# Kernel optimization log

Measured on AMD Instinct MI355X. Metric: run time of the kernel, lower is better.

## Reference

```python
import jax, jax.numpy as jnp
import numpy as np

B, D, H, O, E = 65536, 128, 256, 8, 8  # batch, input_dim, hidden_dim, output_dim, n_phases


def setup_inputs() -> dict:
    key = jax.random.key(0)
    ks = jax.random.split(key, 6)
    scale = 0.05
    x = jax.random.normal(ks[0], (B, D), dtype=jnp.float32)
    phases = jax.random.randint(ks[1], (B,), 0, E, dtype=jnp.int32)
    Ws = jax.random.normal(ks[2], (D, H), dtype=jnp.float32) * scale  # shared Linear weight (transposed)
    bs = jnp.zeros((H,), dtype=jnp.float32)
    W1 = jax.random.normal(ks[3], (E, H, H), dtype=jnp.float32) * scale  # per-head first Linear
    b1 = jnp.zeros((E, H), dtype=jnp.float32)
    W2 = jax.random.normal(ks[4], (E, H, O), dtype=jnp.float32) * scale  # per-head second Linear
    b2 = jnp.zeros((E, O), dtype=jnp.float32)
    return {"x": x, "phases": phases, "Ws": Ws, "bs": bs,
            "W1": W1, "b1": b1, "W2": W2, "b2": b2}


def reference(x, phases, Ws, bs, W1, b1, W2, b2):
    # shared trunk: Linear + ReLU
    h = jax.nn.relu(x @ Ws + bs)                                # [B, H]
    # run every head on every sample (dense grouped GEMM), then gather the
    # per-sample routed head. NOTE: no activation between the two head Linears,
    # matching nn.Sequential(Linear, Linear) in the source.
    h1 = jnp.einsum('bh,ehk->ebk', h, W1) + b1[:, None, :]      # [E, B, H]
    y = jnp.einsum('ebk,eko->ebo', h1, W2) + b2[:, None, :]     # [E, B, O]
    q = y[phases, jnp.arange(x.shape[0])]                       # [B, O] routed select
    return q
```

## Files before the change

### kernel.cpp

```cpp
#include <hip/hip_runtime.h>
#include <hip/hip_bf16.h>
#include <cstdint>


using bf16x8 = __attribute__((ext_vector_type(8))) __bf16;
using f32x4  = __attribute__((ext_vector_type(4))) float;

__device__ __forceinline__ unsigned short bf16b(float f) {
    __bf16 h = (__bf16)f;
    return __builtin_bit_cast(unsigned short, h);
}
__device__ __forceinline__ unsigned pack2(float a, float b) {
    return (unsigned)bf16b(a) | ((unsigned)bf16b(b) << 16);
}

__global__ void prep_kernel(const float* __restrict__ Ws,
                            const float* __restrict__ b1,
                            const float* __restrict__ W1,
                            const float* __restrict__ W2,
                            const float* __restrict__ b2,
                            uint4* __restrict__ wsP,
                            unsigned short* __restrict__ wfP,
                            float* __restrict__ bfuse) {
    const int bid = blockIdx.x, tid = threadIdx.x;
    if (bid < 256) {
        __shared__ float w2sT[8][256];
        const int e = bid >> 5, mc = bid & 31;
        const float* W2e = W2 + (size_t)e * 2048;
        #pragma unroll
        for (int h = 0; h < 2; ++h) {
            int f4 = h * 256 + tid;
            float4 v = ((const float4*)W2e)[f4];
            int k = f4 >> 1, o4 = (f4 & 1) * 4;
            w2sT[o4 + 0][k] = v.x;
            w2sT[o4 + 1][k] = v.y;
            w2sT[o4 + 2][k] = v.z;
            w2sT[o4 + 3][k] = v.w;
        }
        __syncthreads();
        const int mloc = tid >> 5, kg = tid & 31;
        const int m = mc * 8 + mloc;
        const float* w1row = W1 + ((size_t)e * 256 + m) * 256;
        float w1v[8];
        #pragma unroll
        for (int i = 0; i < 8; ++i) w1v[i] = w1row[kg + i * 32];
        float acc[8] = {0,0,0,0,0,0,0,0};
        #pragma unroll
        for (int i = 0; i < 8; ++i) {
            int k = kg + i * 32;
            #pragma unroll
            for (int o = 0; o < 8; ++o) acc[o] += w1v[i] * w2sT[o][k];
        }
        #pragma unroll
        for (int o = 0; o < 8; ++o) {
            acc[o] += __shfl_xor(acc[o], 1);
            acc[o] += __shfl_xor(acc[o], 2);
            acc[o] += __shfl_xor(acc[o], 4);
            acc[o] += __shfl_xor(acc[o], 8);
            acc[o] += __shfl_xor(acc[o], 16);
        }
        if (kg == 0) {
            const int kgf  = m >> 5;
            const int lhif = (m >> 3) & 3;
            const int j    = m & 7;
            #pragma unroll
            for (int o = 0; o < 8; ++o) {
                int c = e * 8 + o;
                int lanef = lhif * 16 + (c & 15);
                int F = (kgf * 4 + (c >> 4)) * 64 + lanef;
                wfP[(size_t)F * 8 + j] = bf16b(acc[o]);
            }
        }
    } else if (bid < 272) {
        const int b2i = bid - 256;
        const int kg = b2i >> 2, hi = b2i & 3;
        const int wv = tid >> 6, lane = tid & 63;
        const int l15 = lane & 15, lhi = lane >> 4;
        const int n  = wv * 64 + hi * 16 + l15;
        const int k0 = kg * 32 + lhi * 8;
        float w[8];
        #pragma unroll
        for (int j = 0; j < 8; ++j)
            w[j] = Ws[(size_t)(k0 + j) * 256 + n];
        uint4 u;
        u.x = pack2(w[0], w[1]); u.y = pack2(w[2], w[3]);
        u.z = pack2(w[4], w[5]); u.w = pack2(w[6], w[7]);
        wsP[((kg * 4 + hi) * 4 + wv) * 64 + lane] = u;
    } else {
        const int e = tid >> 5, l = tid & 31;
        float acc[8] = {0,0,0,0,0,0,0,0};
        #pragma unroll
        for (int i = 0; i < 8; ++i) {
            int k = l * 8 + i;
            float a = b1[e * 256 + k];
            const float* w2r = W2 + ((size_t)(e * 256 + k)) * 8;
            #pragma unroll
            for (int o = 0; o < 8; ++o) acc[o] += a * w2r[o];
        }
        #pragma unroll
        for (int o = 0; o < 8; ++o) {
            acc[o] += __shfl_xor(acc[o], 1);
            acc[o] += __shfl_xor(acc[o], 2);
            acc[o] += __shfl_xor(acc[o], 4);
            acc[o] += __shfl_xor(acc[o], 8);
            acc[o] += __shfl_xor(acc[o], 16);
        }
        if (l == 0) {
            #pragma unroll
            for (int o = 0; o < 8; ++o)
                bfuse[e * 8 + o] = acc[o] + b2[e * 8 + o];
        }
    }
}

__global__ __launch_bounds__(256, 3) void fused_kernel(
    const float* __restrict__ x,
    const int* __restrict__ phases,
    const float* __restrict__ bs,
    const uint4* __restrict__ wsP,
    const uint4* __restrict__ wfP,
    const float* __restrict__ bfuse,
    float* __restrict__ out) {
    __shared__ __align__(16) char lds[49152];
    char* xs = lds;
    char* hs = lds + 16384;

    const int tid = threadIdx.x;
    const int lane = tid & 63;
    const int wv = tid >> 6;
    const int l15 = lane & 15;
    const int lhi = lane >> 4;
    const int row0 = blockIdx.x * 64;

    const float4* xg = (const float4*)x;

    float4 a0[4], d0[4];
    #pragma unroll
    for (int it = 0; it < 4; ++it) {
        int c = it * 256 + tid;
        int row = c >> 4, col8 = c & 15;
        int gi = (row0 + row) * 32 + col8 * 2;
        a0[it] = xg[gi]; d0[it] = xg[gi + 1];
    }
    f32x4 bsv[4];
    #pragma unroll
    for (int hi = 0; hi < 4; ++hi)
        bsv[hi] = *(const f32x4*)(bs + wv * 64 + hi * 16 + lhi * 4);
    const float bfv = bfuse[wv * 16 + l15];
    const int myE = wv * 2 + (l15 >> 3);
    const int co  = l15 & 7;

    #pragma unroll
    for (int it = 0; it < 4; ++it) {
        int c = it * 256 + tid;
        int row = c >> 4, col8 = c & 15;
        unsigned addr = (unsigned)(row * 256 + col8 * 16);
        addr ^= (unsigned)((row & 7) << 4);
        uint4 u;
        u.x = pack2(a0[it].x, a0[it].y); u.y = pack2(a0[it].z, a0[it].w);
        u.z = pack2(d0[it].x, d0[it].y); u.w = pack2(d0[it].z, d0[it].w);
        *(uint4*)(xs + addr) = u;
    }
    __syncthreads();

    f32x4 acc1[4][4];
    #pragma unroll
    for (int hi = 0; hi < 4; ++hi)
        #pragma unroll
        for (int bi = 0; bi < 4; ++bi)
            acc1[hi][bi] = (f32x4){0.f, 0.f, 0.f, 0.f};
    bf16x8 wsCur[4];
    #pragma unroll
    for (int hi = 0; hi < 4; ++hi)
        wsCur[hi] = __builtin_bit_cast(bf16x8, wsP[(hi * 4 + wv) * 64 + lane]);
    #pragma unroll
    for (int kg = 0; kg < 4; ++kg) {
        bf16x8 wsNxt[4];
        if (kg < 3) {
            #pragma unroll
            for (int hi = 0; hi < 4; ++hi)
                wsNxt[hi] = __builtin_bit_cast(bf16x8,
                    wsP[(((kg + 1) * 4 + hi) * 4 + wv) * 64 + lane]);
        }
        bf16x8 xb[4];
        #pragma unroll
        for (int bi = 0; bi < 4; ++bi) {
            int b = bi * 16 + l15;
            unsigned addr = (unsigned)(b * 256 + (kg * 32 + lhi * 8) * 2);
            addr ^= (unsigned)((b & 7) << 4);
            xb[bi] = *(const bf16x8*)(xs + addr);
        }
        __builtin_amdgcn_s_setprio(1);
        #pragma unroll
        for (int hi = 0; hi < 4; ++hi)
            #pragma unroll
            for (int bi = 0; bi < 4; ++bi)
                acc1[hi][bi] = __builtin_amdgcn_mfma_f32_16x16x32_bf16(
                    wsCur[hi], xb[bi], acc1[hi][bi], 0, 0, 0);
        __builtin_amdgcn_s_setprio(0);
        if (kg < 3) {
            #pragma unroll
            for (int hi = 0; hi < 4; ++hi) wsCur[hi] = wsNxt[hi];
        }
    }

    #pragma unroll
    for (int hi = 0; hi < 4; ++hi)
        #pragma unroll
        for (int bi = 0; bi < 4; ++bi) {
            float v0 = acc1[hi][bi][0] + bsv[hi][0]; v0 = v0 > 0.f ? v0 : 0.f;
            float v1 = acc1[hi][bi][1] + bsv[hi][1]; v1 = v1 > 0.f ? v1 : 0.f;
            float v2 = acc1[hi][bi][2] + bsv[hi][2]; v2 = v2 > 0.f ? v2 : 0.f;
            float v3 = acc1[hi][bi][3] + bsv[hi][3]; v3 = v3 > 0.f ? v3 : 0.f;
            uint2 u; u.x = pack2(v0, v1); u.y = pack2(v2, v3);
            int b = bi * 16 + l15;
            int n0 = wv * 64 + hi * 16 + lhi * 4;
            unsigned addr = (unsigned)(b * 512 + n0 * 2);
            addr ^= (unsigned)((b & 7) << 4);
            *(uint2*)(hs + addr) = u;
        }
    bf16x8 wfB[8];
    #pragma unroll
    for (int kg = 0; kg < 8; ++kg)
        wfB[kg] = __builtin_bit_cast(bf16x8, wfP[(kg * 4 + wv) * 64 + lane]);
    __syncthreads();

    f32x4 acc2[4];
    #pragma unroll
    for (int mi = 0; mi < 4; ++mi)
        acc2[mi] = (f32x4){bfv, bfv, bfv, bfv};
    #pragma unroll
    for (int kg = 0; kg < 8; ++kg) {
        bf16x8 ha[4];
        #pragma unroll
        for (int mi = 0; mi < 4; ++mi) {
            int b = mi * 16 + l15;
            unsigned addr = (unsigned)(b * 512 + (kg * 32 + lhi * 8) * 2);
            addr ^= (unsigned)((b & 7) << 4);
            ha[mi] = *(const bf16x8*)(hs + addr);
        }
        __builtin_amdgcn_s_setprio(1);
        #pragma unroll
        for (int mi = 0; mi < 4; ++mi)
            acc2[mi] = __builtin_amdgcn_mfma_f32_16x16x32_bf16(
                ha[mi], wfB[kg], acc2[mi], 0, 0, 0);
        __builtin_amdgcn_s_setprio(0);
    }

    #pragma unroll
    for (int mi = 0; mi < 4; ++mi)
        #pragma unroll
        for (int r = 0; r < 4; ++r) {
            int b = mi * 16 + lhi * 4 + r;
            int e = phases[row0 + b];
            if (e == myE)
                out[(size_t)(row0 + b) * 8 + co] = acc2[mi][r];
        }
}

extern "C" void kernel_launch(void* const* d_in, const int* in_sizes, int n_in,
                              void* d_out, int out_size, void* d_ws, size_t ws_size,
                              hipStream_t stream) {
    const float* x      = (const float*)d_in[0];
    const int*   phases = (const int*)d_in[1];
    const float* Ws     = (const float*)d_in[2];
    const float* bs     = (const float*)d_in[3];
    const float* W1     = (const float*)d_in[4];
    const float* b1     = (const float*)d_in[5];
    const float* W2     = (const float*)d_in[6];
    const float* b2     = (const float*)d_in[7];
    float* out = (float*)d_out;

    uint4*          wsP   = (uint4*)d_ws;
    unsigned short* wfP   = (unsigned short*)((char*)d_ws + 65536);
    float*          bfuse = (float*)((char*)d_ws + 98304);

    prep_kernel<<<273, 256, 0, stream>>>(Ws, b1, W1, W2, b2,
                                         wsP, wfP, bfuse);
    fused_kernel<<<1024, 256, 0, stream>>>(
        x, phases, bs, wsP, (const uint4*)wfP, bfuse, out);
}
```

Measured before the change: 26.19 us.

## Use 768 blocks with two tiles for first 256 blocks and prefetch next x tile

The launch shrinks from 1024 to 768 blocks. The first 256 blocks each process a second 64-row tile (block id + 768), and that tile's x rows are loaded into registers during the first tile's GEMM. The converted bf16 data is then written to LDS before the second GEMM. The intent is to fit the grid into a single residency wave (256 CUs × 3 blocks) and hide global load latency. In exchange the work becomes uneven, since a third of the blocks do double work, and register pressure rises from the extra prefetch buffers.

```diff
diff --git a/kernel.cpp b/kernel.cpp
--- a/kernel.cpp
+++ b/kernel.cpp
@@ -130,17 +130,21 @@
     const int wv = tid >> 6;
     const int l15 = lane & 15;
     const int lhi = lane >> 4;
-    const int row0 = blockIdx.x * 64;
+    const int bid = blockIdx.x;
+    const int nt = (bid < 256) ? 2 : 1;
 
     const float4* xg = (const float4*)x;
 
     float4 a0[4], d0[4];
-    #pragma unroll
-    for (int it = 0; it < 4; ++it) {
-        int c = it * 256 + tid;
-        int row = c >> 4, col8 = c & 15;
-        int gi = (row0 + row) * 32 + col8 * 2;
-        a0[it] = xg[gi]; d0[it] = xg[gi + 1];
+    {
+        int row0 = bid * 64;
+        #pragma unroll
+        for (int it = 0; it < 4; ++it) {
+            int c = it * 256 + tid;
+            int row = c >> 4, col8 = c & 15;
+            int gi = (row0 + row) * 32 + col8 * 2;
+            a0[it] = xg[gi]; d0[it] = xg[gi + 1];
+        }
     }
     f32x4 bsv[4];
     #pragma unroll
@@ -161,101 +165,132 @@
         u.z = pack2(d0[it].x, d0[it].y); u.w = pack2(d0[it].z, d0[it].w);
         *(uint4*)(xs + addr) = u;
     }
-    __syncthreads();
-
-    f32x4 acc1[4][4];
-    #pragma unroll
-    for (int hi = 0; hi < 4; ++hi)
-        #pragma unroll
-        for (int bi = 0; bi < 4; ++bi)
-            acc1[hi][bi] = (f32x4){0.f, 0.f, 0.f, 0.f};
-    bf16x8 wsCur[4];
-    #pragma unroll
-    for (int hi = 0; hi < 4; ++hi)
-        wsCur[hi] = __builtin_bit_cast(bf16x8, wsP[(hi * 4 + wv) * 64 + lane]);
-    #pragma unroll
-    for (int kg = 0; kg < 4; ++kg) {
-        bf16x8 wsNxt[4];
-        if (kg < 3) {
+
+    float4 a1[4], d1[4];
+
+    for (int i = 0; i < nt; ++i) {
+        const int row0 = (i ? bid + 768 : bid) * 64;
+        __syncthreads();
+
+        if (i + 1 < nt) {
+            int nrow0 = (bid + 768) * 64;
+            #pragma unroll
+            for (int it = 0; it < 4; ++it) {
+                int c = it * 256 + tid;
+                int row = c >> 4, col8 = c & 15;
+                int gi = (nrow0 + row) * 32 + col8 * 2;
+                a1[it] = xg[gi]; d1[it] = xg[gi + 1];
+            }
+        }
+
+        f32x4 acc1[4][4];
+        #pragma unroll
+        for (int hi = 0; hi < 4; ++hi)
+            #pragma unroll
+            for (int bi = 0; bi < 4; ++bi)
+                acc1[hi][bi] = (f32x4){0.f, 0.f, 0.f, 0.f};
+        bf16x8 wsCur[4];
+        #pragma unroll
+        for (int hi = 0; hi < 4; ++hi)
+            wsCur[hi] = __builtin_bit_cast(bf16x8, wsP[(hi * 4 + wv) * 64 + lane]);
+        #pragma unroll
+        for (int kg = 0; kg < 4; ++kg) {
+            bf16x8 wsNxt[4];
+            if (kg < 3) {
+                #pragma unroll
+                for (int hi = 0; hi < 4; ++hi)
+                    wsNxt[hi] = __builtin_bit_cast(bf16x8,
+                        wsP[(((kg + 1) * 4 + hi) * 4 + wv) * 64 + lane]);
+            }
+            bf16x8 xb[4];
+            #pragma unroll
+            for (int bi = 0; bi < 4; ++bi) {
+                int b = bi * 16 + l15;
+                unsigned addr = (unsigned)(b * 256 + (kg * 32 + lhi * 8) * 2);
+                addr ^= (unsigned)((b & 7) << 4);
+                xb[bi] = *(const bf16x8*)(xs + addr);
+            }
+            __builtin_amdgcn_s_setprio(1);
             #pragma unroll
             for (int hi = 0; hi < 4; ++hi)
-                wsNxt[hi] = __builtin_bit_cast(bf16x8,
-                    wsP[(((kg + 1) * 4 + hi) * 4 + wv) * 64 + lane]);
-        }
-        bf16x8 xb[4];
-        #pragma unroll
-        for (int bi = 0; bi < 4; ++bi) {
-            int b = bi * 16 + l15;
-            unsigned addr = (unsigned)(b * 256 + (kg * 32 + lhi * 8) * 2);
-            addr ^= (unsigned)((b & 7) << 4);
-            xb[bi] = *(const bf16x8*)(xs + addr);
-        }
-        __builtin_amdgcn_s_setprio(1);
+                #pragma unroll
+                for (int bi = 0; bi < 4; ++bi)
+                    acc1[hi][bi] = __builtin_amdgcn_mfma_f32_16x16x32_bf16(
+                        wsCur[hi], xb[bi], acc1[hi][bi], 0, 0, 0);
+            __builtin_amdgcn_s_setprio(0);
+            if (kg < 3) {
+                #pragma unroll
+                for (int hi = 0; hi < 4; ++hi) wsCur[hi] = wsNxt[hi];
+            }
+        }
+
         #pragma unroll
         for (int hi = 0; hi < 4; ++hi)
             #pragma unroll
-            for (int bi = 0; bi < 4; ++bi)
-                acc1[hi][bi] = __builtin_amdgcn_mfma_f32_16x16x32_bf16(
-                    wsCur[hi], xb[bi], acc1[hi][bi], 0, 0, 0);
-        __builtin_amdgcn_s_setprio(0);
-        if (kg < 3) {
-            #pragma unroll
-            for (int hi = 0; hi < 4; ++hi) wsCur[hi] = wsNxt[hi];
-        }
+            for (int bi = 0; bi < 4; ++bi) {
+                float v0 = acc1[hi][bi][0] + bsv[hi][0]; v0 = v0 > 0.f ? v0 : 0.f;
+                float v1 = acc1[hi][bi][1] + bsv[hi][1]; v1 = v1 > 0.f ? v1 : 0.f;
+                float v2 = acc1[hi][bi][2] + bsv[hi][2]; v2 = v2 > 0.f ? v2 : 0.f;
+                float v3 = acc1[hi][bi][3] + bsv[hi][3]; v3 = v3 > 0.f ? v3 : 0.f;
+                uint2 u; u.x = pack2(v0, v1); u.y = pack2(v2, v3);
+                int b = bi * 16 + l15;
+                int n0 = wv * 64 + hi * 16 + lhi * 4;
+                unsigned addr = (unsigned)(b * 512 + n0 * 2);
+                addr ^= (unsigned)((b & 7) << 4);
+                *(uint2*)(hs + addr) = u;
+            }
+        bf16x8 wfB[8];
+        #pragma unroll
+        for (int kg = 0; kg < 8; ++kg)
+            wfB[kg] = __builtin_bit_cast(bf16x8, wfP[(kg * 4 + wv) * 64 + lane]);
+        __syncthreads();
+
+        if (i + 1 < nt) {
+            #pragma unroll
+            for (int it = 0; it < 4; ++it) {
+                int c = it * 256 + tid;
+                int row = c >> 4, col8 = c & 15;
+                unsigned addr = (unsigned)(row * 256 + col8 * 16);
+                addr ^= (unsigned)((row & 7) << 4);
+                uint4 u;
+                u.x = pack2(a1[it].x, a1[it].y); u.y = pack2(a1[it].z, a1[it].w);
+                u.z = pack2(d1[it].x, d1[it].y); u.w = pack2(d1[it].z, d1[it].w);
+                *(uint4*)(xs + addr) = u;
+            }
+        }
+
+        f32x4 acc2[4];
+        #pragma unroll
+        for (int mi = 0; mi < 4; ++mi)
+            acc2[mi] = (f32x4){bfv, bfv, bfv, bfv};
+        #pragma unroll
+        for (int kg = 0; kg < 8; ++kg) {
+            bf16x8 ha[4];
+            #pragma unroll
+            for (int mi = 0; mi < 4; ++mi) {
+                int b = mi * 16 + l15;
+                unsigned addr = (unsigned)(b * 512 + (kg * 32 + lhi * 8) * 2);
+                addr ^= (unsigned)((b & 7) << 4);
+                ha[mi] = *(const bf16x8*)(hs + addr);
+            }
+            __builtin_amdgcn_s_setprio(1);
+            #pragma unroll
+            for (int mi = 0; mi < 4; ++mi)
+                acc2[mi] = __builtin_amdgcn_mfma_f32_16x16x32_bf16(
+                    ha[mi], wfB[kg], acc2[mi], 0, 0, 0);
+            __builtin_amdgcn_s_setprio(0);
+        }
+
+        #pragma unroll
+        for (int mi = 0; mi < 4; ++mi)
+            #pragma unroll
+            for (int r = 0; r < 4; ++r) {
+                int b = mi * 16 + lhi * 4 + r;
+                int e = phases[row0 + b];
+                if (e == myE)
+                    out[(size_t)(row0 + b) * 8 + co] = acc2[mi][r];
+            }
     }
-
-    #pragma unroll
-    for (int hi = 0; hi < 4; ++hi)
-        #pragma unroll
-        for (int bi = 0; bi < 4; ++bi) {
-            float v0 = acc1[hi][bi][0] + bsv[hi][0]; v0 = v0 > 0.f ? v0 : 0.f;
-            float v1 = acc1[hi][bi][1] + bsv[hi][1]; v1 = v1 > 0.f ? v1 : 0.f;
-            float v2 = acc1[hi][bi][2] + bsv[hi][2]; v2 = v2 > 0.f ? v2 : 0.f;
-            float v3 = acc1[hi][bi][3] + bsv[hi][3]; v3 = v3 > 0.f ? v3 : 0.f;
-            uint2 u; u.x = pack2(v0, v1); u.y = pack2(v2, v3);
-            int b = bi * 16 + l15;
-            int n0 = wv * 64 + hi * 16 + lhi * 4;
-            unsigned addr = (unsigned)(b * 512 + n0 * 2);
-            addr ^= (unsigned)((b & 7) << 4);
-            *(uint2*)(hs + addr) = u;
-        }
-    bf16x8 wfB[8];
-    #pragma unroll
-    for (int kg = 0; kg < 8; ++kg)
-        wfB[kg] = __builtin_bit_cast(bf16x8, wfP[(kg * 4 + wv) * 64 + lane]);
-    __syncthreads();
-
-    f32x4 acc2[4];
-    #pragma unroll
-    for (int mi = 0; mi < 4; ++mi)
-        acc2[mi] = (f32x4){bfv, bfv, bfv, bfv};
-    #pragma unroll
-    for (int kg = 0; kg < 8; ++kg) {
-        bf16x8 ha[4];
-        #pragma unroll
-        for (int mi = 0; mi < 4; ++mi) {
-            int b = mi * 16 + l15;
-            unsigned addr = (unsigned)(b * 512 + (kg * 32 + lhi * 8) * 2);
-            addr ^= (unsigned)((b & 7) << 4);
-            ha[mi] = *(const bf16x8*)(hs + addr);
-        }
-        __builtin_amdgcn_s_setprio(1);
-        #pragma unroll
-        for (int mi = 0; mi < 4; ++mi)
-            acc2[mi] = __builtin_amdgcn_mfma_f32_16x16x32_bf16(
-                ha[mi], wfB[kg], acc2[mi], 0, 0, 0);
-        __builtin_amdgcn_s_setprio(0);
-    }
-
-    #pragma unroll
-    for (int mi = 0; mi < 4; ++mi)
-        #pragma unroll
-        for (int r = 0; r < 4; ++r) {
-            int b = mi * 16 + lhi * 4 + r;
-            int e = phases[row0 + b];
-            if (e == myE)
-                out[(size_t)(row0 + b) * 8 + co] = acc2[mi][r];
-        }
 }
 
 extern "C" void kernel_launch(void* const* d_in, const int* in_sizes, int n_in,
@@ -277,6 +312,6 @@
 
     prep_kernel<<<273, 256, 0, stream>>>(Ws, b1, W1, W2, b2,
                                          wsP, wfP, bfuse);
-    fused_kernel<<<1024, 256, 0, stream>>>(
+    fused_kernel<<<768, 256, 0, stream>>>(
         x, phases, bs, wsP, (const uint4*)wfP, bfuse, out);
 }
```

After: 73.31 us. 180% more time.
